# Optimization experiments

Measured on AMD Instinct MI355X. Metric: run time of the kernel, lower is better.

## Reference

```python
import jax, jax.numpy as jnp
import numpy as np

H = 4          # attention heads
K = 16         # knn neighbors
EPS = 1e-5     # BatchNorm eps


def setup_inputs() -> dict:
    key = jax.random.key(0)
    ks = jax.random.split(key, 10)
    B, C, T, N = 2, 128, 32, 512
    OUT = 128
    HID = 2 * C + 2 * OUT  # ff hidden = in*2 + out*2
    s = 0.02
    return {
        "x_all": jax.random.normal(ks[0], (B, C, T, N), jnp.float32),
        "Wq": jax.random.normal(ks[1], (C, C), jnp.float32) * s,
        "Wk": jax.random.normal(ks[2], (C, C), jnp.float32) * s,
        "Wv": jax.random.normal(ks[3], (C, C), jnp.float32) * s,
        "W1": jax.random.normal(ks[4], (HID, C), jnp.float32) * s,
        "W2": jax.random.normal(ks[5], (OUT, HID), jnp.float32) * s,
        "bn_gamma": 1.0 + 0.1 * jax.random.normal(ks[6], (OUT,), jnp.float32),
        "bn_beta": 0.1 * jax.random.normal(ks[7], (OUT,), jnp.float32),
        "bn_mean": 0.1 * jax.random.normal(ks[8], (OUT,), jnp.float32),
        "bn_var": jax.random.uniform(ks[9], (OUT,), jnp.float32, 0.5, 1.5),
    }


def reference(x_all, Wq, Wk, Wv, W1, W2, bn_gamma, bn_beta, bn_mean, bn_var):
    B, C, T, N = x_all.shape
    D = C // H
    # --- st_group_points: candidate pool = 3 consecutive frames (replicate temporal pad), frame-major ---
    xp = jnp.concatenate([x_all[:, :, :1], x_all, x_all[:, :, -1:]], axis=2)   # (B,C,T+2,N)
    pool = jnp.stack([xp[:, :, :-2], xp[:, :, 1:-1], xp[:, :, 2:]], axis=3)    # (B,C,T,3,N)
    pool = pool.reshape(B, C, T, 3 * N)                                        # (B,C,T,3N)
    # KNN on xyz (channels 0:3); sqrt is monotone so topk on squared dists gives same indices
    a = x_all[:, :3]                                                           # (B,3,T,N)
    b = pool[:, :3]                                                            # (B,3,T,3N)
    d2 = jnp.sum((a[..., :, None] - b[..., None, :]) ** 2, axis=1)             # (B,T,N,3N)
    _, idx = jax.lax.top_k(-d2, K)                                             # (B,T,N,K) smallest-dist
    nb = jnp.take_along_axis(pool[:, :, :, None, :], idx[:, None], axis=-1)    # (B,C,T,N,K)
    rel = x_all[..., None] - nb                                                # diff grouping (B,C,T,N,K)
    # --- per-point local attention over K neighbors (1x1 convs == channel matmuls), all t at once ---
    q = jnp.einsum('oc,bctn->botn', Wq, x_all).reshape(B, H, D, T, N)
    k = jnp.einsum('oc,bctnk->botnk', Wk, rel).reshape(B, H, D, T, N, K)
    v = jnp.einsum('oc,bctnk->botnk', Wv, rel).reshape(B, H, D, T, N, K)
    energy = jnp.einsum('bhdtn,bhdtnk->bhtnk', q, k) / jnp.sqrt(jnp.float32(D))
    attn = jax.nn.softmax(energy, axis=-1)                                     # (B,H,T,N,K)
    agg = jnp.einsum('bhtnk,bhdtnk->bhdtn', attn, v).reshape(B, C, T, N)
    # --- residual + BatchNorm1d (eval mode, running stats) + conv feed-forward ---
    h = x_all + agg
    scale = (bn_gamma / jnp.sqrt(bn_var + EPS))[None, :, None, None]
    h = (h - bn_mean[None, :, None, None]) * scale + bn_beta[None, :, None, None]
    h = jax.nn.leaky_relu(jnp.einsum('oc,bctn->botn', W1, h), 0.2)
    y = jnp.einsum('oc,bctn->botn', W2, h)                                     # (B,OUT,T,N)
    return jnp.concatenate([x_all[:, :4], y], axis=1)                          # (B,4+OUT,T,N)
```

## Files before the change

kernel.cpp:

```cpp
#include <hip/hip_runtime.h>
#include <hip/hip_bf16.h>

typedef __hip_bfloat16 bf16;
typedef unsigned long long u64;
typedef __attribute__((ext_vector_type(8))) short short8;
typedef __attribute__((ext_vector_type(4))) float f32x4;

#define B_   2
#define C_   128
#define T_   32
#define N_   512
#define K_   16
#define HID_ 512
#define TN   (T_*N_)
#define PTS  (B_*T_*N_)

#define MFMA_BF16(a,b,c) __builtin_amdgcn_mfma_f32_16x16x32_bf16((a),(b),(c),0,0,0)

__device__ __forceinline__ float b2f(bf16 v){ return __bfloat162float(v); }
__device__ __forceinline__ bf16  f2b(float v){ return __float2bfloat16(v); }
__device__ __forceinline__ float bqf(short v){
  return __uint_as_float(((unsigned)(unsigned short)v) << 16);
}

__device__ __forceinline__ float ldc(const void* p, int i, bool f32) {
  return f32 ? ((const float*)p)[i] : b2f(((const bf16*)p)[i]);
}

__global__ __launch_bounds__(256) void convw_kernel(
    const void* __restrict__ x,
    const void* wq, const void* wk, const void* wv,
    const void* w1, const void* w2, const void* g, const void* bb,
    const void* m, const void* v,
    bf16* __restrict__ wqb, bf16* __restrict__ wkb, bf16* __restrict__ wvb,
    bf16* __restrict__ w1b, bf16* __restrict__ w2b,
    float* __restrict__ gf, float* __restrict__ bf_, float* __restrict__ mf,
    float* __restrict__ vf, int* __restrict__ flag)
{
  __shared__ int cnt;
  if (threadIdx.x == 0) cnt = 0;
  __syncthreads();
  const unsigned short* u = (const unsigned short*)x;
  int w = 0;
#pragma unroll
  for (int j = 0; j < 8; ++j) {
    unsigned short hv = u[threadIdx.x*8 + j];
    int e = (hv >> 7) & 0xFF;
    if (e >= 0x89) w++;
  }
  if (w) atomicAdd(&cnt, w);
  __syncthreads();
  bool f32 = (cnt > 32);
  if (blockIdx.x == 0 && threadIdx.x == 0) *flag = f32 ? 1 : 0;

  int i = blockIdx.x*256 + threadIdx.x;
  if (i < 16384) { wqb[i] = f2b(ldc(wq, i, f32)); return; } i -= 16384;
  if (i < 16384) { wkb[i] = f2b(ldc(wk, i, f32)); return; } i -= 16384;
  if (i < 16384) { wvb[i] = f2b(ldc(wv, i, f32)); return; } i -= 16384;
  if (i < 65536) { w1b[i] = f2b(ldc(w1, i, f32)); return; } i -= 65536;
  if (i < 65536) { w2b[i] = f2b(ldc(w2, i, f32)); return; } i -= 65536;
  if (i < 128)   { gf[i]  = ldc(g, i, f32); return; }       i -= 128;
  if (i < 128)   { bf_[i] = ldc(bb, i, f32); return; }      i -= 128;
  if (i < 128)   { mf[i]  = ldc(m, i, f32); return; }       i -= 128;
  if (i < 128)   { vf[i]  = ldc(v, i, f32); return; }
}

__device__ __forceinline__ u64 shflx64(u64 v, int m) {
  return (u64)__shfl_xor((long long)v, m, 64);
}

__device__ __forceinline__ void proj_gemm32(const bf16* __restrict__ W,
                                            bf16 (*ys)[136],
                                            const short8 am[2][4],
                                            int mrow, int quad, int ot)
{
  f32x4 acc[2];
#pragma unroll
  for (int mt=0;mt<2;++mt) acc[mt] = (f32x4){0.f,0.f,0.f,0.f};
#pragma unroll
  for (int kq=0;kq<4;++kq) {
    short8 bfr = *(const short8*)&W[(ot*16+mrow)*C_ + kq*32 + quad*8];
#pragma unroll
    for (int mt=0;mt<2;++mt) acc[mt] = MFMA_BF16(am[mt][kq], bfr, acc[mt]);
  }
#pragma unroll
  for (int mt=0;mt<2;++mt)
#pragma unroll
    for (int r=0;r<4;++r)
      ys[mt*16 + quad*4 + r][ot*16 + mrow] = f2b(acc[mt][r]);
}

__device__ __forceinline__ void tile_store32_512(bf16* __restrict__ dst,
                                                 const bf16 (*ys)[136], int tid)
{
  int flat = tid*8;
  int p = flat >> 7, c = flat & 127;
  *(short8*)&dst[(size_t)p*C_ + c] = *(const short8*)&ys[p][c];
}

__global__ __launch_bounds__(512) void projknn_kernel(
    const void* __restrict__ x, const int* __restrict__ flag,
    const bf16* __restrict__ wqb, const bf16* __restrict__ wkb, const bf16* __restrict__ wvb,
    bf16* __restrict__ xTb, bf16* QT, bf16* __restrict__ KT, bf16* __restrict__ VT,
    int* __restrict__ idxout)
{
  __shared__ __align__(16) char smem[28672];
  int tid = threadIdx.x;
  int blk = blockIdx.x;
  int g = blk / 5, r = blk - g*5;
  if (r == 4) {
    bf16 (*xs )[136] = (bf16(*)[136])(smem);
    bf16 (*ysK)[136] = (bf16(*)[136])(smem + 8704);
    bf16 (*ysV)[136] = (bf16(*)[136])(smem + 17408);
    int p0 = g * 32;
    int b = p0 >> 14; int tn0 = p0 & (TN-1);
    if (*flag) {
      const float* xbase = (const float*)x + (size_t)b*C_*TN + tn0;
#pragma unroll
      for (int it=0; it<8; ++it) {
        int i = it*512 + tid;
        int c = i >> 5, p = i & 31;
        xs[p][c] = f2b(xbase[(size_t)c*TN + p]);
      }
    } else {
      const bf16* xbase = (const bf16*)x + (size_t)b*C_*TN + tn0;
#pragma unroll
      for (int it=0; it<8; ++it) {
        int i = it*512 + tid;
        int c = i >> 5, p = i & 31;
        xs[p][c] = xbase[(size_t)c*TN + p];
      }
    }
    __syncthreads();
    tile_store32_512(xTb + (size_t)p0*C_, xs, tid);
    int lane = tid & 63, wave = tid >> 6;
    int mrow = lane & 15, quad = lane >> 4;
    short8 am[2][4];
#pragma unroll
    for (int mt=0;mt<2;++mt)
#pragma unroll
      for (int kq=0;kq<4;++kq)
        am[mt][kq] = *(const short8*)&xs[mt*16 + mrow][kq*32 + quad*8];
    __syncthreads();
    proj_gemm32(wqb, xs,  am, mrow, quad, wave);
    proj_gemm32(wkb, ysK, am, mrow, quad, wave);
    proj_gemm32(wvb, ysV, am, mrow, quad, wave);
    __syncthreads();
    tile_store32_512(QT + (size_t)p0*C_, xs,  tid);
    tile_store32_512(KT + (size_t)p0*C_, ysK, tid);
    tile_store32_512(VT + (size_t)p0*C_, ysV, tid);
  } else {
    float4* cand4 = (float4*)smem;
    u64 (*surv)[64] = (u64(*)[64])(smem + 24576);
    int kblk = g*4 + r;
    int row = kblk >> 6;
    int b = row >> 5, t = row & 31;
    int ng = kblk & 63;
    bool f32 = (*flag != 0);
#pragma unroll
    for (int q = 0; q < 3; ++q) {
      int tt = t - 1 + q; tt = tt < 0 ? 0 : (tt > T_-1 ? T_-1 : tt);
      size_t base = ((size_t)b*C_*T_ + tt)*(size_t)N_ + tid;
      float c0, c1, c2;
      if (f32) {
        const float* xp = (const float*)x;
        c0 = xp[base]; c1 = xp[base + (size_t)T_*N_]; c2 = xp[base + 2*(size_t)T_*N_];
      } else {
        const bf16* xp = (const bf16*)x;
        c0 = b2f(xp[base]); c1 = b2f(xp[base + (size_t)T_*N_]); c2 = b2f(xp[base + 2*(size_t)T_*N_]);
      }
      cand4[q*N_ + tid] = make_float4(c0, c1, c2, 0.f);
    }
    __syncthreads();
    int wave = tid >> 6, lane = tid & 63;
    int n = ng*8 + wave;
    float4 a = cand4[N_ + n];
    unsigned db[24];
#pragma unroll
    for (int j = 0; j < 24; ++j) {
      float4 cm = cand4[lane + (j << 6)];
      float dx = a.x - cm.x;
      float dy = a.y - cm.y;
      float dz = a.z - cm.z;
      float d2 = __fadd_rn(__fadd_rn(__fmul_rn(dx,dx), __fmul_rn(dy,dy)), __fmul_rn(dz,dz));
      db[j] = __float_as_uint(d2);
    }
    unsigned mm[12];
#pragma unroll
    for (int j = 0; j < 12; ++j) mm[j] = db[2*j] < db[2*j+1] ? db[2*j] : db[2*j+1];
#pragma unroll
    for (int j = 0; j < 6; ++j)  mm[j] = mm[2*j] < mm[2*j+1] ? mm[2*j] : mm[2*j+1];
#pragma unroll
    for (int j = 0; j < 3; ++j)  mm[j] = mm[2*j] < mm[2*j+1] ? mm[2*j] : mm[2*j+1];
    unsigned bd = mm[0] < mm[1] ? mm[0] : mm[1];
    bd = bd < mm[2] ? bd : mm[2];
    {
      unsigned lo = 0u, hi = 0x7f800000u;
#pragma unroll
      for (int it = 0; it < 16; ++it) {
        unsigned mid = lo + ((hi - lo) >> 1);
        int cge = __popcll(__ballot(bd <= mid));
        bool ge = (cge >= K_);
        hi = ge ? mid : hi;
        lo = ge ? lo : (mid + 1u);
      }
      bd = hi;
    }
    unsigned U = bd;
    int c = 0;
#pragma unroll
    for (int j = 0; j < 24; ++j) c += (db[j] <= U) ? 1 : 0;
    int ofs = 0, total = 0;
#pragma unroll
    for (int bit = 0; bit < 5; ++bit) {
      u64 mball = __ballot(((c >> bit) & 1) != 0);
      unsigned below = __builtin_amdgcn_mbcnt_hi((unsigned)(mball >> 32),
                        __builtin_amdgcn_mbcnt_lo((unsigned)mball, 0u));
      ofs   += ((int)below) << bit;
      total += (__popcll(mball)) << bit;
    }
    int point = (b*T_ + t)*N_ + n;
    if (total <= 64) {
#pragma unroll
      for (int j = 0; j < 24; ++j) {
        if (db[j] <= U) {
          surv[wave][ofs] = ((u64)db[j] << 11) | (unsigned)(lane + (j << 6));
          ++ofs;
        }
      }
      if (lane == total) surv[wave][lane] = ~0ull;
      __threadfence_block();
      u64 kk = (lane < total) ? surv[wave][lane] : ~0ull;
      int npair = (total + 1) >> 1;
      int rank = 0;
      const ulonglong2* sk2 = (const ulonglong2*)&surv[wave][0];
#pragma unroll 4
      for (int i2 = 0; i2 < npair; ++i2) {
        ulonglong2 kp = sk2[i2];
        rank += (kp.x < kk) ? 1 : 0;
        rank += (kp.y < kk) ? 1 : 0;
      }
      if (rank < K_) idxout[point*K_ + rank] = (int)(kk & 2047u);
    } else {
      u64 key[24];
#pragma unroll
      for (int j = 0; j < 24; ++j)
        key[j] = ((u64)db[j] << 32) | (unsigned)(lane + (j << 6));
      u64 res = ~0ull;
#pragma unroll 1
      for (int rr = 0; rr < 16; ++rr) {
        u64 m2 = key[0];
#pragma unroll
        for (int j = 1; j < 24; ++j) m2 = (key[j] < m2) ? key[j] : m2;
#pragma unroll
        for (int s = 32; s >= 1; s >>= 1) {
          u64 p = shflx64(m2, s);
          m2 = (p < m2) ? p : m2;
        }
        if (lane == rr) res = m2;
        int mwin = (int)(m2 & 0xffffffffu);
        int sel = ((mwin & 63) == lane) ? (mwin >> 6) : -1;
#pragma unroll
        for (int j = 0; j < 24; ++j) if (j == sel) key[j] = ~0ull;
      }
      if (lane < K_) idxout[point*K_ + lane] = (int)(res & 0xffffffffu);
    }
  }
}

__global__ __launch_bounds__(256, 4) void attnmlp_kernel(
    const int* __restrict__ idxin, const bf16* __restrict__ xTb,
    const bf16* __restrict__ QT, const bf16* __restrict__ KT,
    const bf16* __restrict__ VT,
    const float* __restrict__ gf, const float* __restrict__ bf_,
    const float* __restrict__ mf, const float* __restrict__ vf,
    const bf16* __restrict__ w1b, const bf16* __restrict__ w2b,
    const void* __restrict__ x, const int* __restrict__ flag,
    void* __restrict__ out)
{
  __shared__ __align__(16) char smem[31232];
  bf16  (*hTl)[136]       = (bf16 (*)[136])      (smem);
  int   (*colbuf)[K_]     = (int  (*)[K_])       (smem + 8704);
  bf16  (*qbuf)[4][C_]    = (bf16 (*)[4][C_])    (smem + 10752);
  float (*e_lds)[4][K_]   = (float(*)[4][K_])    (smem + 12800);
  bf16  (*vbuf)[K_][136]  = (bf16 (*)[K_][136])  (smem + 13824);
  bf16  (*hidh)[264]      = (bf16 (*)[264])      (smem + 8704);

  int tid = threadIdx.x;
  int gblk = (blockIdx.x & 7)*128 + (blockIdx.x >> 3);
  int p0 = gblk * 32;
  int bb = p0 >> 14;
  int tn0 = p0 & (TN-1);
  bool f32o = (*flag != 0);
  if (tid < 128) {
    int c = tid >> 5, p = tid & 31;
    size_t si = ((size_t)bb*C_ + c)*TN + tn0 + p;
    size_t di = ((size_t)bb*132 + c)*TN + tn0 + p;
    if (f32o) ((float*)out)[di] = ((const float*)x)[si];
    else      ((bf16*)out)[di]  = ((const bf16*)x)[si];
  }

  int tblk = tn0 >> 9;
#pragma unroll
  for (int it = 0; it < 2; ++it) {
    int e = it*256 + tid;
    int row = e >> 4, kk = e & 15;
    int m = idxin[(p0 + row)*K_ + kk];
    int j = m >> 9, nn = m & (N_-1);
    int tt = tblk-1+j; tt = tt<0?0:(tt>T_-1?T_-1:tt);
    colbuf[row][kk] = ((bb*T_ + tt)*N_ + nn)*C_;
  }

  int ppA = tid >> 7, o = tid & 127;
  int ppE = tid >> 6, ke = (tid >> 2) & 15, hde = tid & 3;
  float sc = gf[o] / sqrtf(vf[o] + 1e-5f);
  float smean = mf[o], sbeta = bf_[o];
  float vselfC[2], xselfC[2], vselfN[2], xselfN[2];
  {
    int s0 = (p0 + ppA)*C_;
    int s1 = s0 + 2*C_;
    vselfC[0] = b2f(VT[s0 + o]);  xselfC[0] = b2f(xTb[s0 + o]);
    vselfC[1] = b2f(VT[s1 + o]);  xselfC[1] = b2f(xTb[s1 + o]);
    qbuf[0][ppA][o]     = QT[s0 + o];
    qbuf[0][ppA + 2][o] = QT[s1 + o];
    vselfN[0] = vselfN[1] = xselfN[0] = xselfN[1] = 0.f;
  }
  __syncthreads();
  short8 kv0, kv1, kv2, kv3, vv0, vv1, vv2, vv3;
  {
    int src = colbuf[ppE][ke] + hde*32;
    kv0 = *(const short8*)&KT[src];      kv1 = *(const short8*)&KT[src + 8];
    kv2 = *(const short8*)&KT[src + 16]; kv3 = *(const short8*)&KT[src + 24];
    vv0 = *(const short8*)&VT[src];      vv1 = *(const short8*)&VT[src + 8];
    vv2 = *(const short8*)&VT[src + 16]; vv3 = *(const short8*)&VT[src + 24];
  }
#pragma unroll 1
  for (int sub = 0; sub < 8; ++sub) {
    int cur = sub & 1, nxt = cur ^ 1;
    {
      *(short8*)&vbuf[ppE][ke][hde*32]      = vv0;
      *(short8*)&vbuf[ppE][ke][hde*32 + 8]  = vv1;
      *(short8*)&vbuf[ppE][ke][hde*32 + 16] = vv2;
      *(short8*)&vbuf[ppE][ke][hde*32 + 24] = vv3;
      const bf16* qp = &qbuf[cur][ppE][hde*32];
      short8 q0 = *(const short8*)(qp);
      short8 q1 = *(const short8*)(qp + 8);
      short8 q2 = *(const short8*)(qp + 16);
      short8 q3 = *(const short8*)(qp + 24);
      float e0 = 0.f, e1 = 0.f;
#pragma unroll
      for (int i2=0;i2<8;++i2) e0 = fmaf(bqf(q0[i2]), bqf(kv0[i2]), e0);
#pragma unroll
      for (int i2=0;i2<8;++i2) e0 = fmaf(bqf(q1[i2]), bqf(kv1[i2]), e0);
#pragma unroll
      for (int i2=0;i2<8;++i2) e1 = fmaf(bqf(q2[i2]), bqf(kv2[i2]), e1);
#pragma unroll
      for (int i2=0;i2<8;++i2) e1 = fmaf(bqf(q3[i2]), bqf(kv3[i2]), e1);
      float e = e0 + e1;
      e_lds[ppE][hde][ke] = -e * 0.17677669529663687f;
    }
    if (sub < 7) {
      int row = (sub+1)*4 + ppE;
      int src = colbuf[row][ke] + hde*32;
      kv0 = *(const short8*)&KT[src];      kv1 = *(const short8*)&KT[src + 8];
      kv2 = *(const short8*)&KT[src + 16]; kv3 = *(const short8*)&KT[src + 24];
      vv0 = *(const short8*)&VT[src];      vv1 = *(const short8*)&VT[src + 8];
      vv2 = *(const short8*)&VT[src + 16]; vv3 = *(const short8*)&VT[src + 24];
      int s0 = (p0 + (sub+1)*4 + ppA)*C_;
      int s1 = s0 + 2*C_;
      vselfN[0] = b2f(VT[s0 + o]);  xselfN[0] = b2f(xTb[s0 + o]);
      vselfN[1] = b2f(VT[s1 + o]);  xselfN[1] = b2f(xTb[s1 + o]);
      qbuf[nxt][ppA][o]     = QT[s0 + o];
      qbuf[nxt][ppA + 2][o] = QT[s1 + o];
    }
    __syncthreads();
    {
      int hd2 = o >> 5;
#pragma unroll
      for (int pi = 0; pi < 2; ++pi) {
        int pp = ppA + pi*2;
        float ee[16]; float mx = -3e38f;
#pragma unroll
        for (int kk=0;kk<K_;++kk){ ee[kk]=e_lds[pp][hd2][kk]; mx=fmaxf(mx,ee[kk]); }
        float ssum=0.f;
#pragma unroll
        for (int kk=0;kk<K_;++kk){ ee[kk]=__expf(ee[kk]-mx); ssum+=ee[kk]; }
        float inv = 1.f/ssum;
        float acc = vselfC[pi];
#pragma unroll
        for (int kk=0;kk<K_;++kk)
          acc = fmaf(-(ee[kk]*inv), b2f(vbuf[pp][kk][o]), acc);
        float hv = xselfC[pi] + acc;
        hTl[sub*4 + pp][o] = f2b((hv - smean)*sc + sbeta);
      }
    }
    vselfC[0]=vselfN[0]; vselfC[1]=vselfN[1];
    xselfC[0]=xselfN[0]; xselfC[1]=xselfN[1];
    __syncthreads();
  }

  int lane = tid & 63, wave = tid >> 6;
  int mrow = lane & 15, quad = lane >> 4;
  f32x4 acc2[2][2];
#pragma unroll
  for (int oi=0;oi<2;++oi)
#pragma unroll
    for (int mt=0;mt<2;++mt) acc2[oi][mt] = (f32x4){0.f,0.f,0.f,0.f};

#pragma unroll
  for (int half = 0; half < 2; ++half) {
    if (half) __syncthreads();
    short8 am[2][4];
#pragma unroll
    for (int mt=0;mt<2;++mt)
#pragma unroll
      for (int kq=0;kq<4;++kq)
        am[mt][kq] = *(const short8*)&hTl[mt*16 + mrow][kq*32 + quad*8];
#pragma unroll
    for (int oi = 0; oi < 4; ++oi) {
      int ot_g = half*16 + wave*4 + oi;
      int otl  = wave*4 + oi;
      f32x4 acc[2];
#pragma unroll
      for (int mt=0;mt<2;++mt) acc[mt] = (f32x4){0.f,0.f,0.f,0.f};
#pragma unroll
      for (int kq=0;kq<4;++kq) {
        short8 bfr = *(const short8*)&w1b[(ot_g*16+mrow)*C_ + kq*32 + quad*8];
#pragma unroll
        for (int mt=0;mt<2;++mt) acc[mt] = MFMA_BF16(am[mt][kq], bfr, acc[mt]);
      }
#pragma unroll
      for (int mt=0;mt<2;++mt)
#pragma unroll
        for (int r=0;r<4;++r) {
          float z = acc[mt][r];
          hidh[mt*16 + quad*4 + r][otl*16 + mrow] = f2b(z > 0.f ? z : 0.2f*z);
        }
    }
    __syncthreads();
#pragma unroll
    for (int kc = 0; kc < 4; ++kc) {
      short8 ha[2][2];
#pragma unroll
      for (int mt=0;mt<2;++mt)
#pragma unroll
        for (int kk=0;kk<2;++kk)
          ha[mt][kk] = *(const short8*)&hidh[mt*16 + mrow][(kc*2+kk)*32 + quad*8];
#pragma unroll
      for (int oi=0;oi<2;++oi) {
        int ot2 = wave*2 + oi;
#pragma unroll
        for (int kk=0;kk<2;++kk) {
          int ks_g = half*8 + kc*2 + kk;
          short8 bfr = *(const short8*)&w2b[(ot2*16+mrow)*HID_ + ks_g*32 + quad*8];
#pragma unroll
          for (int mt=0;mt<2;++mt)
            acc2[oi][mt] = MFMA_BF16(ha[mt][kk], bfr, acc2[oi][mt]);
        }
      }
    }
  }
  size_t obase = (size_t)bb*132*TN;
#pragma unroll
  for (int oi=0;oi<2;++oi) {
    int ch = (wave*2+oi)*16 + mrow;
#pragma unroll
    for (int mt=0;mt<2;++mt) {
      int tn = tn0 + mt*16 + quad*4;
      size_t oidx = obase + (size_t)(4+ch)*TN + tn;
      if (f32o) {
        *(f32x4*)&((float*)out)[oidx] = acc2[oi][mt];
      } else {
        bf16 tmp[4];
#pragma unroll
        for (int r=0;r<4;++r) tmp[r] = f2b(acc2[oi][mt][r]);
        *(u64*)&((bf16*)out)[oidx] = *(u64*)tmp;
      }
    }
  }
}

extern "C" void kernel_launch(void* const* d_in, const int* in_sizes, int n_in,
                              void* d_out, int out_size, void* d_ws, size_t ws_size,
                              hipStream_t stream)
{
  (void)in_sizes; (void)n_in; (void)out_size; (void)ws_size;
  const void* x = d_in[0];
  char* ws = (char*)d_ws;
  const size_t MB = (size_t)1<<20;
  bf16*  QT  = (bf16* )(ws + 0*MB);
  bf16*  KT  = (bf16* )(ws + 8*MB);
  bf16*  VT  = (bf16* )(ws + 16*MB);
  bf16*  xTb = (bf16* )(ws + 24*MB);
  int*   idxw= (int*  )(ws + 32*MB);
  bf16*  wqb = (bf16* )(ws + 34*MB);
  bf16*  wkb = (bf16* )(ws + 34*MB + 0x8000);
  bf16*  wvb = (bf16* )(ws + 34*MB + 0x10000);
  bf16*  w1b = (bf16* )(ws + 34*MB + 0x18000);
  bf16*  w2b = (bf16* )(ws + 34*MB + 0x38000);
  float* gf  = (float*)(ws + 34*MB + 0x58000);
  float* bf_ = (float*)(ws + 34*MB + 0x58200);
  float* mf  = (float*)(ws + 34*MB + 0x58400);
  float* vf  = (float*)(ws + 34*MB + 0x58600);
  int*  flag = (int*  )(ws + 34*MB + 0x58800);

  convw_kernel  <<<dim3(706), dim3(256), 0, stream>>>(
      x, d_in[1], d_in[2], d_in[3], d_in[4], d_in[5],
      d_in[6], d_in[7], d_in[8], d_in[9],
      wqb, wkb, wvb, w1b, w2b, gf, bf_, mf, vf, flag);
  projknn_kernel<<<dim3(5120), dim3(512), 0, stream>>>(
      x, flag, wqb, wkb, wvb, xTb, QT, KT, VT, idxw);
  attnmlp_kernel<<<dim3(PTS/32), dim3(256), 0, stream>>>(
      idxw, xTb, QT, KT, VT, gf, bf_, mf, vf, w1b, w2b, x, flag, d_out);
}
```

Before: 190.2 us.

## Make attention phase wave-local to drop per-iteration block barriers

Each wave now handles one point per sub-iteration end to end. It computes the energies, writes its own vbuf/e_lds slice, and does the softmax and aggregation for all 128 channels (two channels per lane). This removes the two __syncthreads per loop iteration and the shared Q double buffer, since Q is now loaded straight into registers from global memory. The cost is more registers for the Q vectors, duplicated softmax work per lane, and reliance on intra-wave ordering of LDS writes and reads with no explicit wave barrier.

```diff
diff --git a/kernel.cpp b/kernel.cpp
--- a/kernel.cpp
+++ b/kernel.cpp
@@ -278,12 +278,11 @@
     const void* __restrict__ x, const int* __restrict__ flag,
     void* __restrict__ out)
 {
-  __shared__ __align__(16) char smem[31232];
+  __shared__ __align__(16) char smem[29184];
   bf16  (*hTl)[136]       = (bf16 (*)[136])      (smem);
   int   (*colbuf)[K_]     = (int  (*)[K_])       (smem + 8704);
-  bf16  (*qbuf)[4][C_]    = (bf16 (*)[4][C_])    (smem + 10752);
-  float (*e_lds)[4][K_]   = (float(*)[4][K_])    (smem + 12800);
-  bf16  (*vbuf)[K_][136]  = (bf16 (*)[K_][136])  (smem + 13824);
+  float (*e_lds)[4][K_]   = (float(*)[4][K_])    (smem + 10752);
+  bf16  (*vbuf)[K_][136]  = (bf16 (*)[K_][136])  (smem + 11776);
   bf16  (*hidh)[264]      = (bf16 (*)[264])      (smem + 8704);
 
   int tid = threadIdx.x;
@@ -311,42 +310,41 @@
     colbuf[row][kk] = ((bb*T_ + tt)*N_ + nn)*C_;
   }
 
-  int ppA = tid >> 7, o = tid & 127;
-  int ppE = tid >> 6, ke = (tid >> 2) & 15, hde = tid & 3;
-  float sc = gf[o] / sqrtf(vf[o] + 1e-5f);
-  float smean = mf[o], sbeta = bf_[o];
-  float vselfC[2], xselfC[2], vselfN[2], xselfN[2];
+  int wv = tid >> 6, lane = tid & 63;
+  int ke = lane >> 2, hde = lane & 3;
+  int o1 = lane, o2 = lane + 64;
+  int hda = o1 >> 5, hdb = o2 >> 5;
+  float sc1 = gf[o1] / sqrtf(vf[o1] + 1e-5f);
+  float sc2 = gf[o2] / sqrtf(vf[o2] + 1e-5f);
+  float sm1 = mf[o1], sm2 = mf[o2];
+  float sb1 = bf_[o1], sb2 = bf_[o2];
+  __syncthreads();
+
+  short8 kv0, kv1, kv2, kv3, vv0, vv1, vv2, vv3, q0, q1, q2, q3;
+  float vs1, vs2, xs1, xs2;
   {
-    int s0 = (p0 + ppA)*C_;
-    int s1 = s0 + 2*C_;
-    vselfC[0] = b2f(VT[s0 + o]);  xselfC[0] = b2f(xTb[s0 + o]);
-    vselfC[1] = b2f(VT[s1 + o]);  xselfC[1] = b2f(xTb[s1 + o]);
-    qbuf[0][ppA][o]     = QT[s0 + o];
-    qbuf[0][ppA + 2][o] = QT[s1 + o];
-    vselfN[0] = vselfN[1] = xselfN[0] = xselfN[1] = 0.f;
-  }
-  __syncthreads();
-  short8 kv0, kv1, kv2, kv3, vv0, vv1, vv2, vv3;
-  {
-    int src = colbuf[ppE][ke] + hde*32;
+    int row = wv;
+    int src = colbuf[row][ke] + hde*32;
     kv0 = *(const short8*)&KT[src];      kv1 = *(const short8*)&KT[src + 8];
     kv2 = *(const short8*)&KT[src + 16]; kv3 = *(const short8*)&KT[src + 24];
     vv0 = *(const short8*)&VT[src];      vv1 = *(const short8*)&VT[src + 8];
     vv2 = *(const short8*)&VT[src + 16]; vv3 = *(const short8*)&VT[src + 24];
+    int self = (p0 + row)*C_;
+    q0 = *(const short8*)&QT[self + hde*32];
+    q1 = *(const short8*)&QT[self + hde*32 + 8];
+    q2 = *(const short8*)&QT[self + hde*32 + 16];
+    q3 = *(const short8*)&QT[self + hde*32 + 24];
+    vs1 = b2f(VT[self + o1]);  vs2 = b2f(VT[self + o2]);
+    xs1 = b2f(xTb[self + o1]); xs2 = b2f(xTb[self + o2]);
   }
 #pragma unroll 1
   for (int sub = 0; sub < 8; ++sub) {
-    int cur = sub & 1, nxt = cur ^ 1;
+    int row = sub*4 + wv;
     {
-      *(short8*)&vbuf[ppE][ke][hde*32]      = vv0;
-      *(short8*)&vbuf[ppE][ke][hde*32 + 8]  = vv1;
-      *(short8*)&vbuf[ppE][ke][hde*32 + 16] = vv2;
-      *(short8*)&vbuf[ppE][ke][hde*32 + 24] = vv3;
-      const bf16* qp = &qbuf[cur][ppE][hde*32];
-      short8 q0 = *(const short8*)(qp);
-      short8 q1 = *(const short8*)(qp + 8);
-      short8 q2 = *(const short8*)(qp + 16);
-      short8 q3 = *(const short8*)(qp + 24);
+      *(short8*)&vbuf[wv][ke][hde*32]      = vv0;
+      *(short8*)&vbuf[wv][ke][hde*32 + 8]  = vv1;
+      *(short8*)&vbuf[wv][ke][hde*32 + 16] = vv2;
+      *(short8*)&vbuf[wv][ke][hde*32 + 24] = vv3;
       float e0 = 0.f, e1 = 0.f;
 #pragma unroll
       for (int i2=0;i2<8;++i2) e0 = fmaf(bqf(q0[i2]), bqf(kv0[i2]), e0);
@@ -357,49 +355,57 @@
 #pragma unroll
       for (int i2=0;i2<8;++i2) e1 = fmaf(bqf(q3[i2]), bqf(kv3[i2]), e1);
       float e = e0 + e1;
-      e_lds[ppE][hde][ke] = -e * 0.17677669529663687f;
-    }
+      e_lds[wv][hde][ke] = -e * 0.17677669529663687f;
+    }
+    float cvs1 = vs1, cvs2 = vs2, cxs1 = xs1, cxs2 = xs2;
     if (sub < 7) {
-      int row = (sub+1)*4 + ppE;
-      int src = colbuf[row][ke] + hde*32;
+      int nrow = row + 4;
+      int src = colbuf[nrow][ke] + hde*32;
       kv0 = *(const short8*)&KT[src];      kv1 = *(const short8*)&KT[src + 8];
       kv2 = *(const short8*)&KT[src + 16]; kv3 = *(const short8*)&KT[src + 24];
       vv0 = *(const short8*)&VT[src];      vv1 = *(const short8*)&VT[src + 8];
       vv2 = *(const short8*)&VT[src + 16]; vv3 = *(const short8*)&VT[src + 24];
-      int s0 = (p0 + (sub+1)*4 + ppA)*C_;
-      int s1 = s0 + 2*C_;
-      vselfN[0] = b2f(VT[s0 + o]);  xselfN[0] = b2f(xTb[s0 + o]);
-      vselfN[1] = b2f(VT[s1 + o]);  xselfN[1] = b2f(xTb[s1 + o]);
-      qbuf[nxt][ppA][o]     = QT[s0 + o];
-      qbuf[nxt][ppA + 2][o] = QT[s1 + o];
-    }
-    __syncthreads();
+      int self = (p0 + nrow)*C_;
+      q0 = *(const short8*)&QT[self + hde*32];
+      q1 = *(const short8*)&QT[self + hde*32 + 8];
+      q2 = *(const short8*)&QT[self + hde*32 + 16];
+      q3 = *(const short8*)&QT[self + hde*32 + 24];
+      vs1 = b2f(VT[self + o1]);  vs2 = b2f(VT[self + o2]);
+      xs1 = b2f(xTb[self + o1]); xs2 = b2f(xTb[self + o2]);
+    }
     {
-      int hd2 = o >> 5;
-#pragma unroll
-      for (int pi = 0; pi < 2; ++pi) {
-        int pp = ppA + pi*2;
-        float ee[16]; float mx = -3e38f;
-#pragma unroll
-        for (int kk=0;kk<K_;++kk){ ee[kk]=e_lds[pp][hd2][kk]; mx=fmaxf(mx,ee[kk]); }
-        float ssum=0.f;
-#pragma unroll
-        for (int kk=0;kk<K_;++kk){ ee[kk]=__expf(ee[kk]-mx); ssum+=ee[kk]; }
-        float inv = 1.f/ssum;
-        float acc = vselfC[pi];
-#pragma unroll
-        for (int kk=0;kk<K_;++kk)
-          acc = fmaf(-(ee[kk]*inv), b2f(vbuf[pp][kk][o]), acc);
-        float hv = xselfC[pi] + acc;
-        hTl[sub*4 + pp][o] = f2b((hv - smean)*sc + sbeta);
-      }
-    }
-    vselfC[0]=vselfN[0]; vselfC[1]=vselfN[1];
-    xselfC[0]=xselfN[0]; xselfC[1]=xselfN[1];
-    __syncthreads();
-  }
-
-  int lane = tid & 63, wave = tid >> 6;
+      float ee[16]; float mx = -3e38f;
+#pragma unroll
+      for (int kk=0;kk<K_;++kk){ ee[kk]=e_lds[wv][hda][kk]; mx=fmaxf(mx,ee[kk]); }
+      float ssum=0.f;
+#pragma unroll
+      for (int kk=0;kk<K_;++kk){ ee[kk]=__expf(ee[kk]-mx); ssum+=ee[kk]; }
+      float inv = 1.f/ssum;
+      float acc = cvs1;
+#pragma unroll
+      for (int kk=0;kk<K_;++kk)
+        acc = fmaf(-(ee[kk]*inv), b2f(vbuf[wv][kk][o1]), acc);
+      float hv = cxs1 + acc;
+      hTl[row][o1] = f2b((hv - sm1)*sc1 + sb1);
+    }
+    {
+      float ee[16]; float mx = -3e38f;
+#pragma unroll
+      for (int kk=0;kk<K_;++kk){ ee[kk]=e_lds[wv][hdb][kk]; mx=fmaxf(mx,ee[kk]); }
+      float ssum=0.f;
+#pragma unroll
+      for (int kk=0;kk<K_;++kk){ ee[kk]=__expf(ee[kk]-mx); ssum+=ee[kk]; }
+      float inv = 1.f/ssum;
+      float acc = cvs2;
+#pragma unroll
+      for (int kk=0;kk<K_;++kk)
+        acc = fmaf(-(ee[kk]*inv), b2f(vbuf[wv][kk][o2]), acc);
+      float hv = cxs2 + acc;
+      hTl[row][o2] = f2b((hv - sm2)*sc2 + sb2);
+    }
+  }
+  __syncthreads();
+
   int mrow = lane & 15, quad = lane >> 4;
   f32x4 acc2[2][2];
 #pragma unroll
@@ -418,8 +424,8 @@
         am[mt][kq] = *(const short8*)&hTl[mt*16 + mrow][kq*32 + quad*8];
 #pragma unroll
     for (int oi = 0; oi < 4; ++oi) {
-      int ot_g = half*16 + wave*4 + oi;
-      int otl  = wave*4 + oi;
+      int ot_g = half*16 + wv*4 + oi;
+      int otl  = wv*4 + oi;
       f32x4 acc[2];
 #pragma unroll
       for (int mt=0;mt<2;++mt) acc[mt] = (f32x4){0.f,0.f,0.f,0.f};
@@ -448,7 +454,7 @@
           ha[mt][kk] = *(const short8*)&hidh[mt*16 + mrow][(kc*2+kk)*32 + quad*8];
 #pragma unroll
       for (int oi=0;oi<2;++oi) {
-        int ot2 = wave*2 + oi;
+        int ot2 = wv*2 + oi;
 #pragma unroll
         for (int kk=0;kk<2;++kk) {
           int ks_g = half*8 + kc*2 + kk;
@@ -463,7 +469,7 @@
   size_t obase = (size_t)bb*132*TN;
 #pragma unroll
   for (int oi=0;oi<2;++oi) {
-    int ch = (wave*2+oi)*16 + mrow;
+    int ch = (wv*2+oi)*16 + mrow;
 #pragma unroll
     for (int mt=0;mt<2;++mt) {
       int tn = tn0 + mt*16 + quad*4;
```

After: 192.0 us. Within noise of the previous version (+0.9%).
